# Kernel optimization log

Hardware: AMD Instinct MI355X
Metric: run time of the kernel (lower is better)

## Reference

```python
import jax, jax.numpy as jnp
import numpy as np
from jax import lax

FEATURE_SIZES = (19, 38, 76)   # 608px YOLOv3 grids
NUM_CLASSES = 80
THR_CONF = 0.5
THR_NMS = 0.3
K = 300                        # max detections kept per image (padded, fixed shape)
EPS = 1e-7


def setup_inputs() -> dict:
    key = jax.random.key(0)
    k1, k2 = jax.random.split(key)
    B = 32
    N = sum(f * f * 3 for f in FEATURE_SIZES)  # 22743
    p_yolo = jax.random.normal(k1, (B, N, 5 + NUM_CLASSES), dtype=jnp.float32)
    # normalized anchor xywh table, kept safely inside (0,1)
    ancs = jax.random.uniform(k2, (N, 4), dtype=jnp.float32, minval=0.05, maxval=0.95)
    # fsize_p = np.repeat(feature_sizes, grid^2*3) as in the torch forward
    fs = np.concatenate([np.full((f * f * 3, 2), f, dtype=np.float32) for f in FEATURE_SIZES], axis=0)
    return {"p_yolo": p_yolo, "ancs": ancs, "fsize_p": jnp.asarray(fs)}


def _iou_matrix(b):
    # b: [K,4] ltrb -> [K,K] pairwise IoU
    area = jnp.maximum(b[:, 2] - b[:, 0], 0.0) * jnp.maximum(b[:, 3] - b[:, 1], 0.0)
    lt = jnp.maximum(b[:, None, :2], b[None, :, :2])
    rb = jnp.minimum(b[:, None, 2:], b[None, :, 2:])
    wh = jnp.maximum(rb - lt, 0.0)
    inter = wh[..., 0] * wh[..., 1]
    return inter / (area[:, None] + area[None, :] - inter + EPS)


def _greedy_nms(iou, valid):
    # iou: [K,K] (rows sorted by descending score), valid: [K] bool
    def body(keep, i):
        suppressed = jnp.any((iou[i] > THR_NMS) & keep)
        k_i = valid[i] & jnp.logical_not(suppressed)
        return keep.at[i].set(k_i), k_i
    keep, _ = lax.scan(body, jnp.zeros(valid.shape[0], dtype=bool), jnp.arange(valid.shape[0]))
    return keep


def reference(p_yolo, ancs, fsize_p):
    # sigmoid_(p[:,:,4:])
    conf = jax.nn.sigmoid(p_yolo[..., 4])          # [B,N]
    cls = jax.nn.sigmoid(p_yolo[..., 5:])          # [B,N,C]
    # fix_boxes4yolo3: xy = sigmoid(txy)/fsize + anc_xy ; wh = exp(twh)*anc_wh
    xy = jax.nn.sigmoid(p_yolo[..., :2]) / fsize_p + ancs[..., :2]
    wh = jnp.exp(p_yolo[..., 2:4]) * ancs[..., 2:]
    ltrb = jnp.concatenate([xy - wh * 0.5, xy + wh * 0.5], axis=-1)  # xywh2ltrb, [B,N,4]
    labels = jnp.argmax(cls, axis=-1) + 1                            # [B,N] int

    valid = conf > THR_CONF
    scores_m = jnp.where(valid, conf, 0.0)
    top_scores, idx = lax.top_k(scores_m, K)                         # [B,K], sorted desc
    boxes_k = jnp.take_along_axis(ltrb, idx[..., None], axis=1)      # [B,K,4]
    labels_k = jnp.take_along_axis(labels, idx, axis=1)              # [B,K]
    valid_k = top_scores > THR_CONF

    # label-aware NMS: offset boxes per class (label_nms semantics); coords live in ~[-1,2]
    boxes_off = boxes_k + labels_k.astype(boxes_k.dtype)[..., None] * 4.0
    iou = jax.vmap(_iou_matrix)(boxes_off)                           # [B,K,K]
    keep = jax.vmap(_greedy_nms)(iou, valid_k)                       # [B,K] bool

    B = p_yolo.shape[0]
    ids_batch = jnp.broadcast_to(jnp.arange(B, dtype=jnp.int32)[:, None], (B, K))
    scores_out = top_scores * keep.astype(top_scores.dtype)          # 0 for suppressed/pad
    labels_out = labels_k * keep.astype(labels_k.dtype)
    return ids_batch, boxes_k, labels_out, scores_out
```

## Files before the change

kernel.cpp:

```cpp
#include <hip/hip_runtime.h>
#include <hip/hip_bf16.h>

#pragma clang fp contract(off)

#define BATCH 32
#define NPOS  22743
#define ROW   85
#define KTOP  300
#define KPAD  512

#define OFF_IDS    0
#define OFF_BOXES  (BATCH*KTOP)
#define OFF_LABELS (OFF_BOXES + BATCH*KTOP*4)
#define OFF_SCORES (OFF_LABELS + BATCH*KTOP)

#define WS_KEYS   0
#define WS_SELIDX (BATCH*NPOS*4)
#define WS_SELKEY (WS_SELIDX + BATCH*KTOP*4)
#define WS_LABELS (WS_SELKEY + BATCH*KTOP*4)

__device__ __forceinline__ float sigmoidf_ref(float x) {
    return 1.0f / (1.0f + expf(-x));
}

__global__ __launch_bounds__(256) void k_extract(const float* __restrict__ p,
                                                 unsigned* __restrict__ keys) {
    const int g = blockIdx.x * 256 + threadIdx.x;
    if (g < BATCH * NPOS) {
        float x = p[(size_t)g * ROW + 4];
        float cf = sigmoidf_ref(x);
        keys[g] = (cf > 0.5f) ? (__float_as_uint(cf) & 0x00FFFFFFu) : 0u;
    }
}

__global__ __launch_bounds__(256) void k_select(const unsigned* __restrict__ keys,
                                                int* __restrict__ sel_idx,
                                                unsigned* __restrict__ sel_key) {
    const int b = blockIdx.x;
    const int t = threadIdx.x;
    __shared__ unsigned h[256];
    __shared__ unsigned sc[256];
    __shared__ unsigned bcast_bin, bcast_R;
    __shared__ int cnt, ovf;
    __shared__ unsigned long long arr[KPAD];
    const unsigned* kb = keys + (size_t)b * NPOS;

    unsigned prefix = 0;
    unsigned R = KTOP;

    for (int pass = 0; pass < 3; ++pass) {
        const int shift = 16 - 8 * pass;
        h[t] = 0;
        __syncthreads();
        for (int n = t; n < NPOS; n += 256) {
            unsigned u = kb[n];
            if (pass == 0 || (u >> (shift + 8)) == prefix)
                atomicAdd(&h[(u >> shift) & 255], 1u);
        }
        __syncthreads();
        sc[t] = h[t];
        __syncthreads();
        for (int off = 1; off < 256; off <<= 1) {
            unsigned add = (t + off < 256) ? sc[t + off] : 0u;
            __syncthreads();
            sc[t] += add;
            __syncthreads();
        }
        unsigned snext = (t < 255) ? sc[t + 1] : 0u;
        if (sc[t] >= R && snext < R) { bcast_bin = (unsigned)t; bcast_R = R - snext; }
        __syncthreads();
        prefix = (prefix << 8) | bcast_bin;
        R = bcast_R;
        __syncthreads();
    }
    const unsigned T = prefix;

    if (t == 0) { cnt = 0; ovf = 0; }
    for (int e = t; e < KPAD; e += 256) arr[e] = 0ull;
    __syncthreads();
    for (int n = t; n < NPOS; n += 256) {
        unsigned u = kb[n];
        if (u >= T) {
            int pos = atomicAdd(&cnt, 1);
            if (pos < KPAD) arr[pos] = ((unsigned long long)u << 32) | (unsigned)(~n);
            else ovf = 1;
        }
    }
    __syncthreads();
    if (ovf) {
        if (t == 0) cnt = 0;
        __syncthreads();
        for (int e = t; e < KPAD; e += 256) arr[e] = 0ull;
        __syncthreads();
        for (int n = t; n < NPOS; n += 256) {
            unsigned u = kb[n];
            if (u > T) {
                int pos = atomicAdd(&cnt, 1);
                if (pos < KPAD) arr[pos] = ((unsigned long long)u << 32) | (unsigned)(~n);
            }
        }
        __syncthreads();
        if (t == 0) {
            int c = min(cnt, KPAD - 1);
            for (int n = 0; n < NPOS && c < KTOP; ++n)
                if (kb[n] == T) arr[c++] = ((unsigned long long)T << 32) | (unsigned)(~n);
        }
        __syncthreads();
    }
    for (unsigned kk = 2; kk <= KPAD; kk <<= 1)
        for (unsigned j = kk >> 1; j > 0; j >>= 1) {
            __syncthreads();
            for (unsigned e = t; e < KPAD; e += 256) {
                unsigned partner = e ^ j;
                if (partner > e) {
                    bool up = ((e & kk) == 0);
                    unsigned long long a = arr[e], bb = arr[partner];
                    if (up ? (a > bb) : (a < bb)) { arr[e] = bb; arr[partner] = a; }
                }
            }
        }
    __syncthreads();
    for (int e = t; e < KTOP; e += 256) {
        unsigned long long v = arr[KPAD - 1 - e];
        sel_idx[b * KTOP + e] = (int)(~(unsigned)v);
        sel_key[b * KTOP + e] = (unsigned)(v >> 32);
    }
}

__global__ __launch_bounds__(256) void k_decode(const float* __restrict__ p,
                                                const float* __restrict__ ancs,
                                                const float* __restrict__ fsz,
                                                const int* __restrict__ sel_idx,
                                                int* __restrict__ labels,
                                                float* __restrict__ out) {
    const int wid = (int)((blockIdx.x * blockDim.x + threadIdx.x) >> 6);
    const int lane = threadIdx.x & 63;
    if (wid >= BATCH * KTOP) return;
    const int b = wid / KTOP, k = wid % KTOP;
    const int n = sel_idx[b * KTOP + k];
    const size_t base = ((size_t)b * NPOS + n) * ROW;

    float v1 = p[base + lane];
    float v2 = (lane < 21) ? p[base + 64 + lane] : -INFINITY;

    float bv = -INFINITY; int bc = 1 << 20;
    if (lane >= 5) { bv = v1; bc = lane - 5; }
    if (lane < 21) {
        int c2 = 59 + lane;
        if (v2 > bv || (v2 == bv && c2 < bc)) { bv = v2; bc = c2; }
    }
    for (int d = 32; d; d >>= 1) {
        float ov = __shfl_xor(bv, d);
        int   oc = __shfl_xor(bc, d);
        if (ov > bv || (ov == bv && oc < bc)) { bv = ov; bc = oc; }
    }
    const int label = bc + 1;

    float t0 = __shfl(v1, 0), t1 = __shfl(v1, 1), t2 = __shfl(v1, 2), t3 = __shfl(v1, 3);
    if (lane == 0) {
        float f0 = fsz[(size_t)n * 2 + 0], f1 = fsz[(size_t)n * 2 + 1];
        float a0 = ancs[(size_t)n * 4 + 0], a1 = ancs[(size_t)n * 4 + 1];
        float a2 = ancs[(size_t)n * 4 + 2], a3 = ancs[(size_t)n * 4 + 3];
        float cx = sigmoidf_ref(t0) / f0 + a0;
        float cy = sigmoidf_ref(t1) / f1 + a1;
        float w  = expf(t2) * a2;
        float hh = expf(t3) * a3;
        float* ob = out + OFF_BOXES + (size_t)(b * KTOP + k) * 4;
        ob[0] = cx - w * 0.5f;
        ob[1] = cy - hh * 0.5f;
        ob[2] = cx + w * 0.5f;
        ob[3] = cy + hh * 0.5f;
        out[OFF_IDS + b * KTOP + k] = (float)b;
        labels[b * KTOP + k] = label;
    }
}

__global__ __launch_bounds__(256) void k_nms(const float* __restrict__ boxes,
                                             const int* __restrict__ labels,
                                             const unsigned* __restrict__ sel_key,
                                             float* __restrict__ out) {
    const int b = blockIdx.x, t = threadIdx.x;
    __shared__ float bx[KTOP][4];
    __shared__ float area[KTOP];
    __shared__ float score[KTOP];
    __shared__ int   lab[KTOP];
    __shared__ int   validb[KTOP];
    __shared__ unsigned long long O[KTOP * 5];
    __shared__ unsigned long long vb[5];
    __shared__ unsigned long long kw[5];

    for (int k = t; k < KTOP; k += 256) {
        const float* p4 = boxes + (size_t)(b * KTOP + k) * 4;
        int L = labels[b * KTOP + k];
        float off = (float)L * 4.0f;
        float l = p4[0] + off, tp = p4[1] + off, r = p4[2] + off, bt = p4[3] + off;
        bx[k][0] = l; bx[k][1] = tp; bx[k][2] = r; bx[k][3] = bt;
        area[k] = fmaxf(r - l, 0.0f) * fmaxf(bt - tp, 0.0f);
        lab[k] = L;
        unsigned key = sel_key[b * KTOP + k];
        validb[k] = (key != 0u) ? 1 : 0;
        score[k] = __uint_as_float(key | 0x3F000000u);
    }
    __syncthreads();

    for (int i = t; i < KTOP; i += 256) {
        float li = bx[i][0], ti = bx[i][1], ri = bx[i][2], bi = bx[i][3], ai = area[i];
        for (int q = 0; q < 5; ++q) {
            unsigned long long wq = 0ull;
            int j0 = q * 64, j1 = min(i, j0 + 64);
            for (int j = j0; j < j1; ++j) {
                float lt0 = fmaxf(li, bx[j][0]);
                float lt1 = fmaxf(ti, bx[j][1]);
                float rb0 = fminf(ri, bx[j][2]);
                float rb1 = fminf(bi, bx[j][3]);
                float ww = fmaxf(rb0 - lt0, 0.0f);
                float hh = fmaxf(rb1 - lt1, 0.0f);
                float inter = ww * hh;
                float iou = inter / (((ai + area[j]) - inter) + 1e-7f);
                if (iou > 0.3f) wq |= 1ull << (j & 63);
            }
            O[i * 5 + q] = wq;
        }
    }
    if (t < 5) {
        unsigned long long v = 0ull;
        for (int j = 0; j < 64; ++j) {
            int idx = t * 64 + j;
            if (idx < KTOP && validb[idx]) v |= 1ull << j;
        }
        vb[t] = v;
    }
    __syncthreads();

    if (t < 64) {
        const int lane = t;
        unsigned long long kwl = 0ull;
        unsigned long long vbl = (lane < 5) ? vb[lane] : 0ull;
        unsigned long long cur = (lane < 5) ? O[lane] : 0ull;
        for (int i = 0; i < KTOP; ++i) {
            unsigned long long nxt = (lane < 5 && i < KTOP - 1) ? O[(i + 1) * 5 + lane] : 0ull;
            bool sup = __any((cur & kwl) != 0ull);
            if (lane == (i >> 6)) {
                bool v = (vbl >> (i & 63)) & 1ull;
                if (v && !sup) kwl |= 1ull << (i & 63);
            }
            cur = nxt;
        }
        if (lane < 5) kw[lane] = kwl;
    }
    __syncthreads();

    for (int k = t; k < KTOP; k += 256) {
        bool kp = (kw[k >> 6] >> (k & 63)) & 1ull;
        out[OFF_SCORES + b * KTOP + k] = kp ? score[k] : 0.0f;
        out[OFF_LABELS + b * KTOP + k] = kp ? (float)lab[k] : 0.0f;
    }
}

extern "C" void kernel_launch(void* const* d_in, const int* in_sizes, int n_in,
                              void* d_out, int out_size, void* d_ws, size_t ws_size,
                              hipStream_t stream) {
    const float* p    = (const float*)d_in[0];
    const float* ancs = (const float*)d_in[1];
    const float* fsz  = (const float*)d_in[2];
    float* out = (float*)d_out;

    char* w = (char*)d_ws;
    unsigned* keys    = (unsigned*)(w + WS_KEYS);
    int*      sel_idx = (int*)(w + WS_SELIDX);
    unsigned* sel_key = (unsigned*)(w + WS_SELKEY);
    int*      labels  = (int*)(w + WS_LABELS);

    const int total = BATCH * NPOS;
    hipLaunchKernelGGL(k_extract, dim3((total + 255) / 256), dim3(256), 0, stream, p, keys);
    hipLaunchKernelGGL(k_select, dim3(BATCH), dim3(256), 0, stream, keys, sel_idx, sel_key);
    hipLaunchKernelGGL(k_decode, dim3((BATCH * KTOP + 3) / 4), dim3(256), 0, stream,
                       p, ancs, fsz, sel_idx, labels, out);
    hipLaunchKernelGGL(k_nms, dim3(BATCH), dim3(256), 0, stream, out + OFF_BOXES, labels, sel_key, out);
}
```

Baseline: 453.9 us.

## Vectorize radix select, skip zero-key atomics, and parallelize NMS IoU with ballots

Pads the per-image key array to a multiple of four so the radix-select passes can read keys as uint4 with 512 threads per block. Zero keys, which are the common case, are now counted per thread and reduced across the wave instead of each hitting a shared-memory atomic on bin 0. The NMS IoU mask build moves from one thread per row looping over columns to one wave per row, with each lane testing one column and __ballot forming the 64-bit mask. The valid bitmask is likewise built by ballot. Together these target the serialized atomics in the select kernel and the long per-thread loops in NMS, at the cost of extra padding and larger blocks.

```diff
diff --git a/kernel.cpp b/kernel.cpp
--- a/kernel.cpp
+++ b/kernel.cpp
@@ -5,6 +5,8 @@
 
 #define BATCH 32
 #define NPOS  22743
+#define NPOSP 22744
+#define N4P   (NPOSP/4)
 #define ROW   85
 #define KTOP  300
 #define KPAD  512
@@ -15,7 +17,7 @@
 #define OFF_SCORES (OFF_LABELS + BATCH*KTOP)
 
 #define WS_KEYS   0
-#define WS_SELIDX (BATCH*NPOS*4)
+#define WS_SELIDX (BATCH*NPOSP*4)
 #define WS_SELKEY (WS_SELIDX + BATCH*KTOP*4)
 #define WS_LABELS (WS_SELKEY + BATCH*KTOP*4)
 
@@ -25,49 +27,68 @@
 
 __global__ __launch_bounds__(256) void k_extract(const float* __restrict__ p,
                                                  unsigned* __restrict__ keys) {
-    const int g = blockIdx.x * 256 + threadIdx.x;
-    if (g < BATCH * NPOS) {
-        float x = p[(size_t)g * ROW + 4];
+    const int n = blockIdx.x * 256 + threadIdx.x;
+    const int b = blockIdx.y;
+    if (n < NPOS) {
+        float x = p[((size_t)b * NPOS + n) * ROW + 4];
         float cf = sigmoidf_ref(x);
-        keys[g] = (cf > 0.5f) ? (__float_as_uint(cf) & 0x00FFFFFFu) : 0u;
-    }
-}
-
-__global__ __launch_bounds__(256) void k_select(const unsigned* __restrict__ keys,
+        keys[(size_t)b * NPOSP + n] = (cf > 0.5f) ? (__float_as_uint(cf) & 0x00FFFFFFu) : 0u;
+    } else if (n < NPOSP) {
+        keys[(size_t)b * NPOSP + n] = 0u;
+    }
+}
+
+__global__ __launch_bounds__(512) void k_select(const unsigned* __restrict__ keys,
                                                 int* __restrict__ sel_idx,
                                                 unsigned* __restrict__ sel_key) {
     const int b = blockIdx.x;
     const int t = threadIdx.x;
+    const int lane = t & 63;
     __shared__ unsigned h[256];
     __shared__ unsigned sc[256];
     __shared__ unsigned bcast_bin, bcast_R;
     __shared__ int cnt, ovf;
     __shared__ unsigned long long arr[KPAD];
-    const unsigned* kb = keys + (size_t)b * NPOS;
+    const unsigned* kb = keys + (size_t)b * NPOSP;
+    const uint4* kb4 = reinterpret_cast<const uint4*>(kb);
 
     unsigned prefix = 0;
     unsigned R = KTOP;
 
     for (int pass = 0; pass < 3; ++pass) {
         const int shift = 16 - 8 * pass;
-        h[t] = 0;
-        __syncthreads();
-        for (int n = t; n < NPOS; n += 256) {
-            unsigned u = kb[n];
-            if (pass == 0 || (u >> (shift + 8)) == prefix)
-                atomicAdd(&h[(u >> shift) & 255], 1u);
-        }
-        __syncthreads();
-        sc[t] = h[t];
+        if (t < 256) h[t] = 0;
+        __syncthreads();
+        int zc = 0;
+        for (int i4 = t; i4 < N4P; i4 += 512) {
+            uint4 u4 = kb4[i4];
+            unsigned uu[4] = {u4.x, u4.y, u4.z, u4.w};
+            #pragma unroll
+            for (int c = 0; c < 4; ++c) {
+                unsigned u = uu[c];
+                bool match = (pass == 0) || ((u >> (shift + 8)) == prefix);
+                if (match) {
+                    if (u) atomicAdd(&h[(u >> shift) & 255], 1u);
+                    else   ++zc;
+                }
+            }
+        }
+        #pragma unroll
+        for (int d = 32; d; d >>= 1) zc += __shfl_xor(zc, d);
+        if (lane == 0 && zc) atomicAdd(&h[0], (unsigned)zc);
+        __syncthreads();
+        if (t < 256) sc[t] = h[t];
         __syncthreads();
         for (int off = 1; off < 256; off <<= 1) {
-            unsigned add = (t + off < 256) ? sc[t + off] : 0u;
+            unsigned add = (t < 256 && t + off < 256) ? sc[t + off] : 0u;
             __syncthreads();
-            sc[t] += add;
+            if (t < 256) sc[t] += add;
             __syncthreads();
         }
-        unsigned snext = (t < 255) ? sc[t + 1] : 0u;
-        if (sc[t] >= R && snext < R) { bcast_bin = (unsigned)t; bcast_R = R - snext; }
+        if (t < 256) {
+            unsigned snext = (t < 255) ? sc[t + 1] : 0u;
+            if (sc[t] >= R && snext < R) { bcast_bin = (unsigned)t; bcast_R = R - snext; }
+        }
         __syncthreads();
         prefix = (prefix << 8) | bcast_bin;
         R = bcast_R;
@@ -76,23 +97,29 @@
     const unsigned T = prefix;
 
     if (t == 0) { cnt = 0; ovf = 0; }
-    for (int e = t; e < KPAD; e += 256) arr[e] = 0ull;
-    __syncthreads();
-    for (int n = t; n < NPOS; n += 256) {
-        unsigned u = kb[n];
-        if (u >= T) {
-            int pos = atomicAdd(&cnt, 1);
-            if (pos < KPAD) arr[pos] = ((unsigned long long)u << 32) | (unsigned)(~n);
-            else ovf = 1;
+    for (int e = t; e < KPAD; e += 512) arr[e] = 0ull;
+    __syncthreads();
+    for (int i4 = t; i4 < N4P; i4 += 512) {
+        uint4 u4 = kb4[i4];
+        unsigned uu[4] = {u4.x, u4.y, u4.z, u4.w};
+        #pragma unroll
+        for (int c = 0; c < 4; ++c) {
+            unsigned u = uu[c];
+            if (u >= T) {
+                int n = i4 * 4 + c;
+                int pos = atomicAdd(&cnt, 1);
+                if (pos < KPAD) arr[pos] = ((unsigned long long)u << 32) | (unsigned)(~n);
+                else ovf = 1;
+            }
         }
     }
     __syncthreads();
     if (ovf) {
         if (t == 0) cnt = 0;
         __syncthreads();
-        for (int e = t; e < KPAD; e += 256) arr[e] = 0ull;
-        __syncthreads();
-        for (int n = t; n < NPOS; n += 256) {
+        for (int e = t; e < KPAD; e += 512) arr[e] = 0ull;
+        __syncthreads();
+        for (int n = t; n < NPOS; n += 512) {
             unsigned u = kb[n];
             if (u > T) {
                 int pos = atomicAdd(&cnt, 1);
@@ -110,20 +137,18 @@
     for (unsigned kk = 2; kk <= KPAD; kk <<= 1)
         for (unsigned j = kk >> 1; j > 0; j >>= 1) {
             __syncthreads();
-            for (unsigned e = t; e < KPAD; e += 256) {
-                unsigned partner = e ^ j;
-                if (partner > e) {
-                    bool up = ((e & kk) == 0);
-                    unsigned long long a = arr[e], bb = arr[partner];
-                    if (up ? (a > bb) : (a < bb)) { arr[e] = bb; arr[partner] = a; }
-                }
-            }
-        }
-    __syncthreads();
-    for (int e = t; e < KTOP; e += 256) {
-        unsigned long long v = arr[KPAD - 1 - e];
-        sel_idx[b * KTOP + e] = (int)(~(unsigned)v);
-        sel_key[b * KTOP + e] = (unsigned)(v >> 32);
+            unsigned e = (unsigned)t, partner = e ^ j;
+            if (partner > e) {
+                bool up = ((e & kk) == 0);
+                unsigned long long a = arr[e], bb = arr[partner];
+                if (up ? (a > bb) : (a < bb)) { arr[e] = bb; arr[partner] = a; }
+            }
+        }
+    __syncthreads();
+    if (t < KTOP) {
+        unsigned long long v = arr[KPAD - 1 - t];
+        sel_idx[b * KTOP + t] = (int)(~(unsigned)v);
+        sel_key[b * KTOP + t] = (unsigned)(v >> 32);
     }
 }
 
@@ -175,65 +200,66 @@
     }
 }
 
-__global__ __launch_bounds__(256) void k_nms(const float* __restrict__ boxes,
+__global__ __launch_bounds__(512) void k_nms(const float* __restrict__ boxes,
                                              const int* __restrict__ labels,
                                              const unsigned* __restrict__ sel_key,
                                              float* __restrict__ out) {
     const int b = blockIdx.x, t = threadIdx.x;
-    __shared__ float bx[KTOP][4];
-    __shared__ float area[KTOP];
-    __shared__ float score[KTOP];
-    __shared__ int   lab[KTOP];
-    __shared__ int   validb[KTOP];
+    const int lane = t & 63, wave = t >> 6;
+    __shared__ float4 bx4[KTOP];
+    __shared__ float  area_s[KTOP];
+    __shared__ float  score_s[KTOP];
+    __shared__ int    lab_s[KTOP];
     __shared__ unsigned long long O[KTOP * 5];
     __shared__ unsigned long long vb[5];
     __shared__ unsigned long long kw[5];
 
-    for (int k = t; k < KTOP; k += 256) {
-        const float* p4 = boxes + (size_t)(b * KTOP + k) * 4;
-        int L = labels[b * KTOP + k];
+    bool valid = false;
+    if (t < KTOP) {
+        const float* p4 = boxes + (size_t)(b * KTOP + t) * 4;
+        int L = labels[b * KTOP + t];
         float off = (float)L * 4.0f;
         float l = p4[0] + off, tp = p4[1] + off, r = p4[2] + off, bt = p4[3] + off;
-        bx[k][0] = l; bx[k][1] = tp; bx[k][2] = r; bx[k][3] = bt;
-        area[k] = fmaxf(r - l, 0.0f) * fmaxf(bt - tp, 0.0f);
-        lab[k] = L;
-        unsigned key = sel_key[b * KTOP + k];
-        validb[k] = (key != 0u) ? 1 : 0;
-        score[k] = __uint_as_float(key | 0x3F000000u);
-    }
-    __syncthreads();
-
-    for (int i = t; i < KTOP; i += 256) {
-        float li = bx[i][0], ti = bx[i][1], ri = bx[i][2], bi = bx[i][3], ai = area[i];
+        bx4[t] = make_float4(l, tp, r, bt);
+        area_s[t] = fmaxf(r - l, 0.0f) * fmaxf(bt - tp, 0.0f);
+        lab_s[t] = L;
+        unsigned key = sel_key[b * KTOP + t];
+        valid = (key != 0u);
+        score_s[t] = __uint_as_float(key | 0x3F000000u);
+    }
+    unsigned long long vbw = __ballot(valid);
+    if (lane == 0 && wave < 5) vb[wave] = vbw;
+    __syncthreads();
+
+    for (int i = wave; i < KTOP; i += 8) {
+        float4 bi = bx4[i];
+        float  ai = area_s[i];
+        int qmax = (i + 63) >> 6;
         for (int q = 0; q < 5; ++q) {
-            unsigned long long wq = 0ull;
-            int j0 = q * 64, j1 = min(i, j0 + 64);
-            for (int j = j0; j < j1; ++j) {
-                float lt0 = fmaxf(li, bx[j][0]);
-                float lt1 = fmaxf(ti, bx[j][1]);
-                float rb0 = fminf(ri, bx[j][2]);
-                float rb1 = fminf(bi, bx[j][3]);
-                float ww = fmaxf(rb0 - lt0, 0.0f);
-                float hh = fmaxf(rb1 - lt1, 0.0f);
-                float inter = ww * hh;
-                float iou = inter / (((ai + area[j]) - inter) + 1e-7f);
-                if (iou > 0.3f) wq |= 1ull << (j & 63);
-            }
-            O[i * 5 + q] = wq;
-        }
-    }
-    if (t < 5) {
-        unsigned long long v = 0ull;
-        for (int j = 0; j < 64; ++j) {
-            int idx = t * 64 + j;
-            if (idx < KTOP && validb[idx]) v |= 1ull << j;
-        }
-        vb[t] = v;
+            unsigned long long w = 0ull;
+            if (q < qmax) {
+                int j = q * 64 + lane;
+                bool pred = false;
+                if (j < i) {
+                    float4 bj = bx4[j];
+                    float lt0 = fmaxf(bi.x, bj.x);
+                    float lt1 = fmaxf(bi.y, bj.y);
+                    float rb0 = fminf(bi.z, bj.z);
+                    float rb1 = fminf(bi.w, bj.w);
+                    float ww = fmaxf(rb0 - lt0, 0.0f);
+                    float hh = fmaxf(rb1 - lt1, 0.0f);
+                    float inter = ww * hh;
+                    float iou = inter / (((ai + area_s[j]) - inter) + 1e-7f);
+                    pred = iou > 0.3f;
+                }
+                w = __ballot(pred);
+            }
+            if (lane == 0) O[i * 5 + q] = w;
+        }
     }
     __syncthreads();
 
     if (t < 64) {
-        const int lane = t;
         unsigned long long kwl = 0ull;
         unsigned long long vbl = (lane < 5) ? vb[lane] : 0ull;
         unsigned long long cur = (lane < 5) ? O[lane] : 0ull;
@@ -250,10 +276,10 @@
     }
     __syncthreads();
 
-    for (int k = t; k < KTOP; k += 256) {
-        bool kp = (kw[k >> 6] >> (k & 63)) & 1ull;
-        out[OFF_SCORES + b * KTOP + k] = kp ? score[k] : 0.0f;
-        out[OFF_LABELS + b * KTOP + k] = kp ? (float)lab[k] : 0.0f;
+    if (t < KTOP) {
+        bool kp = (kw[t >> 6] >> (t & 63)) & 1ull;
+        out[OFF_SCORES + b * KTOP + t] = kp ? score_s[t] : 0.0f;
+        out[OFF_LABELS + b * KTOP + t] = kp ? (float)lab_s[t] : 0.0f;
     }
 }
 
@@ -271,10 +297,9 @@
     unsigned* sel_key = (unsigned*)(w + WS_SELKEY);
     int*      labels  = (int*)(w + WS_LABELS);
 
-    const int total = BATCH * NPOS;
-    hipLaunchKernelGGL(k_extract, dim3((total + 255) / 256), dim3(256), 0, stream, p, keys);
-    hipLaunchKernelGGL(k_select, dim3(BATCH), dim3(256), 0, stream, keys, sel_idx, sel_key);
+    hipLaunchKernelGGL(k_extract, dim3((NPOSP + 255) / 256, BATCH), dim3(256), 0, stream, p, keys);
+    hipLaunchKernelGGL(k_select, dim3(BATCH), dim3(512), 0, stream, keys, sel_idx, sel_key);
     hipLaunchKernelGGL(k_decode, dim3((BATCH * KTOP + 3) / 4), dim3(256), 0, stream,
                        p, ancs, fsz, sel_idx, labels, out);
-    hipLaunchKernelGGL(k_nms, dim3(BATCH), dim3(256), 0, stream, out + OFF_BOXES, labels, sel_key, out);
-}
+    hipLaunchKernelGGL(k_nms, dim3(BATCH), dim3(512), 0, stream, out + OFF_BOXES, labels, sel_key, out);
+}
```

Result: faster. 385.2 us (-15.1%).
